# Kernel tuning notes

Hardware: AMD Instinct MI355X
Metric: run time of the kernel (lower is better)

Reference implementation:

```python
import jax, jax.numpy as jnp
import numpy as np

GAMMA = 0.99
LMBDA = 0.95
SHAPE = (8192, 256, 4, 1)  # (batch, steps, agents, 1)


def setup_inputs() -> dict:
    key = jax.random.key(0)
    k1, k2, k3, k4 = jax.random.split(key, 4)
    reward = jax.random.normal(k1, SHAPE, dtype=jnp.float32)
    # sparse binary termination flags (as float, matching terminated.float())
    terminated = (jax.random.uniform(k2, SHAPE) < 0.01).astype(jnp.float32)
    value = jax.random.normal(k3, SHAPE, dtype=jnp.float32)
    next_value = jax.random.normal(k4, SHAPE, dtype=jnp.float32)
    return {"reward": reward, "terminated": terminated,
            "value": value, "next_value": next_value}


def _gae(reward, terminated, value, next_value):
    not_done = 1.0 - terminated
    # delta_t = r_t + gamma * V(s_{t+1}) * not_done_t - V(s_t), all steps at once
    delta = reward + GAMMA * next_value * not_done - value  # (B, T, ...)

    # time-major for the scan: (T, B, ...)
    delta_t = jnp.moveaxis(delta, 1, 0)
    nd_t = jnp.moveaxis(not_done, 1, 0)

    def step(gae, x):
        d, nd = x
        gae = d + GAMMA * LMBDA * nd * gae
        return gae, gae

    init = jnp.zeros(delta_t.shape[1:], dtype=delta.dtype)
    # reverse=True: backward-time recurrence, outputs aligned to original order
    _, adv_t = jax.lax.scan(step, init, (delta_t, nd_t), reverse=True)
    advantages = jnp.moveaxis(adv_t, 0, 1)  # back to (B, T, ...)
    returns = advantages + value
    return advantages, returns


def reference(reward, terminated, value, next_value):
    return _gae(reward, terminated, value, next_value)
```

## Files before the change

### kernel.cpp

```cpp
#include <hip/hip_runtime.h>


#define GAMMA 0.99f
#define LMBDA 0.95f

typedef float f32x4 __attribute__((ext_vector_type(4)));
typedef unsigned char u8;

constexpr float K0 = GAMMA * LMBDA;

__device__ __forceinline__ void issue_loads(
    const f32x4* __restrict__ R4, const f32x4* __restrict__ T4,
    const f32x4* __restrict__ V4, const f32x4* __restrict__ N4,
    int b, int lane, f32x4 r[4], f32x4 tm[4], f32x4 v[4], f32x4 nv[4])
{
#pragma unroll
    for (int q = 0; q < 4; ++q) {
        const int gi = b * 256 + 64 * q + lane;
        r[q]  = R4[gi];
        tm[q] = T4[gi];
        v[q]  = V4[gi];
        nv[q] = N4[gi];
    }
}

__device__ __forceinline__ void phaseA(
    float* __restrict__ D_, u8* __restrict__ C_, int lane,
    const f32x4 r[4], const f32x4 tm[4], const f32x4 nv[4], const f32x4 v[4])
{
#pragma unroll
    for (int q = 0; q < 4; ++q) {
        const int f    = 64 * q + lane;
        const int s    = 255 - f;
        const int row  = s & 15;
        const int col  = (4 * (s >> 4) + 4 * row) & 63;
        const int addr = row * 64 + col;

        f32x4 d4;
        d4.x = r[q].x + GAMMA * nv[q].x * (1.0f - tm[q].x) - v[q].x;
        d4.y = r[q].y + GAMMA * nv[q].y * (1.0f - tm[q].y) - v[q].y;
        d4.z = r[q].z + GAMMA * nv[q].z * (1.0f - tm[q].z) - v[q].z;
        d4.w = r[q].w + GAMMA * nv[q].w * (1.0f - tm[q].w) - v[q].w;
        const unsigned pk = (tm[q].x == 0.0f ? 0x00000001u : 0u)
                          | (tm[q].y == 0.0f ? 0x00000100u : 0u)
                          | (tm[q].z == 0.0f ? 0x00010000u : 0u)
                          | (tm[q].w == 0.0f ? 0x01000000u : 0u);
        *((f32x4*)&D_[addr])    = d4;
        *((unsigned*)&C_[addr]) = pk;
    }
}

__device__ __forceinline__ void scan_store(
    float* __restrict__ D_, const u8* __restrict__ C_,
    int lane, int b, const f32x4 v4[4],
    f32x4* __restrict__ adv4, f32x4* __restrict__ ret4)
{
    asm volatile("s_waitcnt lgkmcnt(0)" ::: "memory");

    const int tc = lane >> 2;
    const int a  = lane & 3;

    float d[16];
    unsigned mask = 0;
#pragma unroll
    for (int j = 0; j < 16; ++j) {
        const int col = (4 * tc + 4 * j + a) & 63;
        d[j] = D_[j * 64 + col];
        mask |= ((unsigned)C_[j * 64 + col]) << j;
    }

    float D = d[0];
    float K = (mask & 1u) ? K0 : 0.0f;
#pragma unroll
    for (int j = 1; j < 16; ++j) {
        const float cj = ((mask >> j) & 1u) ? K0 : 0.0f;
        D = d[j] + cj * D;
        K = cj * K;
    }

#pragma unroll
    for (int s2 = 1; s2 < 16; s2 <<= 1) {
        const float pD = __shfl_up(D, (unsigned)(4 * s2), 64);
        const float pK = __shfl_up(K, (unsigned)(4 * s2), 64);
        if (tc >= s2) { D = D + K * pD; K = K * pK; }
    }

    float x = __shfl_up(D, 4u, 64);
    if (tc == 0) x = 0.0f;

    float g = x;
#pragma unroll
    for (int j = 0; j < 16; ++j) {
        const float cj = ((mask >> j) & 1u) ? K0 : 0.0f;
        g = d[j] + cj * g;
        const int col = (4 * tc + 4 * j + a) & 63;
        D_[j * 64 + col] = g;
    }
    asm volatile("s_waitcnt lgkmcnt(0)" ::: "memory");

#pragma unroll
    for (int q = 0; q < 4; ++q) {
        const int f   = 64 * q + lane;
        const int s   = 255 - f;
        const int row = s & 15;
        const int col = (4 * (s >> 4) + 4 * row) & 63;
        const f32x4 g4 = *((const f32x4*)&D_[row * 64 + col]);

        const int gi = b * 256 + f;
        adv4[gi] = g4;
        ret4[gi] = g4 + v4[q];
    }
    asm volatile("" ::: "memory");
}

__global__ __launch_bounds__(256, 2) void gae_scan_kernel(
    const float* __restrict__ reward,
    const float* __restrict__ terminated,
    const float* __restrict__ value,
    const float* __restrict__ next_value,
    float* __restrict__ adv_out,
    float* __restrict__ ret_out)
{
    __shared__ float bufD[4][16 * 64];
    __shared__ u8    bufC[4][16 * 64];

    const int w    = threadIdx.x >> 6;
    const int lane = threadIdx.x & 63;
    const int wv   = blockIdx.x * 4 + w;

    float* __restrict__ D_ = bufD[w];
    u8*    __restrict__ C_ = bufC[w];

    const f32x4* R4 = (const f32x4*)reward;
    const f32x4* T4 = (const f32x4*)terminated;
    const f32x4* V4 = (const f32x4*)value;
    const f32x4* N4 = (const f32x4*)next_value;
    f32x4* adv4 = (f32x4*)adv_out;
    f32x4* ret4 = (f32x4*)ret_out;

    f32x4 r[2][4], tm[2][4], v[2][4], nv[2][4];

    issue_loads(R4, T4, V4, N4, wv, lane, r[0], tm[0], v[0], nv[0]);

#pragma unroll
    for (int g = 0; g < 4; ++g) {
        const int cb = g & 1;
        const int nb = cb ^ 1;
        const int b  = g * 2048 + wv;

        phaseA(D_, C_, lane, r[cb], tm[cb], nv[cb], v[cb]);

        if (g < 3) {
            issue_loads(R4, T4, V4, N4, b + 2048, lane,
                        r[nb], tm[nb], v[nb], nv[nb]);
        }

        scan_store(D_, C_, lane, b, v[cb], adv4, ret4);
    }
}

extern "C" void kernel_launch(void* const* d_in, const int* in_sizes, int n_in,
                              void* d_out, int out_size, void* d_ws, size_t ws_size,
                              hipStream_t stream) {
    const float* reward     = (const float*)d_in[0];
    const float* terminated = (const float*)d_in[1];
    const float* value      = (const float*)d_in[2];
    const float* next_value = (const float*)d_in[3];

    const int B = 8192;
    const int n_elem = B * 256 * 4;
    float* adv = (float*)d_out;
    float* ret = adv + n_elem;

    gae_scan_kernel<<<512, 256, 0, stream>>>(reward, terminated, value,
                                             next_value, adv, ret);
}
```

Baseline: 176.5 us.

## Split each sequence's time scan across two wavefronts with a shared-memory carry

Each batch sequence is now handled by two wavefronts, each owning half of the 256 time steps, instead of one wavefront scanning all of them. The later-time half hands its aggregate carry to the earlier half through shared memory after a block barrier. The grid doubles to 1024 blocks and launch bounds ask for 4 blocks per CU. Per-wave register and LDS use is halved to raise occupancy and memory-level parallelism, at the cost of a block-wide barrier per iteration and an extra carry exchange.

Measured after the change: 178.2 us. No clear change (+1.0%).

```diff
diff --git a/kernel.cpp b/kernel.cpp
--- a/kernel.cpp
+++ b/kernel.cpp
@@ -9,111 +9,7 @@
 
 constexpr float K0 = GAMMA * LMBDA;
 
-__device__ __forceinline__ void issue_loads(
-    const f32x4* __restrict__ R4, const f32x4* __restrict__ T4,
-    const f32x4* __restrict__ V4, const f32x4* __restrict__ N4,
-    int b, int lane, f32x4 r[4], f32x4 tm[4], f32x4 v[4], f32x4 nv[4])
-{
-#pragma unroll
-    for (int q = 0; q < 4; ++q) {
-        const int gi = b * 256 + 64 * q + lane;
-        r[q]  = R4[gi];
-        tm[q] = T4[gi];
-        v[q]  = V4[gi];
-        nv[q] = N4[gi];
-    }
-}
-
-__device__ __forceinline__ void phaseA(
-    float* __restrict__ D_, u8* __restrict__ C_, int lane,
-    const f32x4 r[4], const f32x4 tm[4], const f32x4 nv[4], const f32x4 v[4])
-{
-#pragma unroll
-    for (int q = 0; q < 4; ++q) {
-        const int f    = 64 * q + lane;
-        const int s    = 255 - f;
-        const int row  = s & 15;
-        const int col  = (4 * (s >> 4) + 4 * row) & 63;
-        const int addr = row * 64 + col;
-
-        f32x4 d4;
-        d4.x = r[q].x + GAMMA * nv[q].x * (1.0f - tm[q].x) - v[q].x;
-        d4.y = r[q].y + GAMMA * nv[q].y * (1.0f - tm[q].y) - v[q].y;
-        d4.z = r[q].z + GAMMA * nv[q].z * (1.0f - tm[q].z) - v[q].z;
-        d4.w = r[q].w + GAMMA * nv[q].w * (1.0f - tm[q].w) - v[q].w;
-        const unsigned pk = (tm[q].x == 0.0f ? 0x00000001u : 0u)
-                          | (tm[q].y == 0.0f ? 0x00000100u : 0u)
-                          | (tm[q].z == 0.0f ? 0x00010000u : 0u)
-                          | (tm[q].w == 0.0f ? 0x01000000u : 0u);
-        *((f32x4*)&D_[addr])    = d4;
-        *((unsigned*)&C_[addr]) = pk;
-    }
-}
-
-__device__ __forceinline__ void scan_store(
-    float* __restrict__ D_, const u8* __restrict__ C_,
-    int lane, int b, const f32x4 v4[4],
-    f32x4* __restrict__ adv4, f32x4* __restrict__ ret4)
-{
-    asm volatile("s_waitcnt lgkmcnt(0)" ::: "memory");
-
-    const int tc = lane >> 2;
-    const int a  = lane & 3;
-
-    float d[16];
-    unsigned mask = 0;
-#pragma unroll
-    for (int j = 0; j < 16; ++j) {
-        const int col = (4 * tc + 4 * j + a) & 63;
-        d[j] = D_[j * 64 + col];
-        mask |= ((unsigned)C_[j * 64 + col]) << j;
-    }
-
-    float D = d[0];
-    float K = (mask & 1u) ? K0 : 0.0f;
-#pragma unroll
-    for (int j = 1; j < 16; ++j) {
-        const float cj = ((mask >> j) & 1u) ? K0 : 0.0f;
-        D = d[j] + cj * D;
-        K = cj * K;
-    }
-
-#pragma unroll
-    for (int s2 = 1; s2 < 16; s2 <<= 1) {
-        const float pD = __shfl_up(D, (unsigned)(4 * s2), 64);
-        const float pK = __shfl_up(K, (unsigned)(4 * s2), 64);
-        if (tc >= s2) { D = D + K * pD; K = K * pK; }
-    }
-
-    float x = __shfl_up(D, 4u, 64);
-    if (tc == 0) x = 0.0f;
-
-    float g = x;
-#pragma unroll
-    for (int j = 0; j < 16; ++j) {
-        const float cj = ((mask >> j) & 1u) ? K0 : 0.0f;
-        g = d[j] + cj * g;
-        const int col = (4 * tc + 4 * j + a) & 63;
-        D_[j * 64 + col] = g;
-    }
-    asm volatile("s_waitcnt lgkmcnt(0)" ::: "memory");
-
-#pragma unroll
-    for (int q = 0; q < 4; ++q) {
-        const int f   = 64 * q + lane;
-        const int s   = 255 - f;
-        const int row = s & 15;
-        const int col = (4 * (s >> 4) + 4 * row) & 63;
-        const f32x4 g4 = *((const f32x4*)&D_[row * 64 + col]);
-
-        const int gi = b * 256 + f;
-        adv4[gi] = g4;
-        ret4[gi] = g4 + v4[q];
-    }
-    asm volatile("" ::: "memory");
-}
-
-__global__ __launch_bounds__(256, 2) void gae_scan_kernel(
+__global__ __launch_bounds__(256, 4) void gae_scan_kernel(
     const float* __restrict__ reward,
     const float* __restrict__ terminated,
     const float* __restrict__ value,
@@ -121,12 +17,15 @@
     float* __restrict__ adv_out,
     float* __restrict__ ret_out)
 {
-    __shared__ float bufD[4][16 * 64];
-    __shared__ u8    bufC[4][16 * 64];
+    __shared__ float bufD[4][8 * 64];
+    __shared__ u8    bufC[4][8 * 64];
+    __shared__ float carryBuf[2][2][4];
 
     const int w    = threadIdx.x >> 6;
     const int lane = threadIdx.x & 63;
-    const int wv   = blockIdx.x * 4 + w;
+    const int sl   = w >> 1;
+    const int h    = w & 1;
+    const int tb   = (1 - h) * 128;
 
     float* __restrict__ D_ = bufD[w];
     u8*    __restrict__ C_ = bufC[w];
@@ -138,24 +37,127 @@
     f32x4* adv4 = (f32x4*)adv_out;
     f32x4* ret4 = (f32x4*)ret_out;
 
-    f32x4 r[2][4], tm[2][4], v[2][4], nv[2][4];
+    const int tc = lane >> 2;
+    const int a  = lane & 3;
 
-    issue_loads(R4, T4, V4, N4, wv, lane, r[0], tm[0], v[0], nv[0]);
+    const int seq0 = blockIdx.x * 2 + sl;
+
+    f32x4 r[2][2], tm[2][2], v[2][2], nv[2][2];
+
+#pragma unroll
+    for (int q = 0; q < 2; ++q) {
+        const int gi = seq0 * 256 + tb + 64 * q + lane;
+        r[0][q]  = R4[gi];
+        tm[0][q] = T4[gi];
+        v[0][q]  = V4[gi];
+        nv[0][q] = N4[gi];
+    }
 
 #pragma unroll
     for (int g = 0; g < 4; ++g) {
         const int cb = g & 1;
         const int nb = cb ^ 1;
-        const int b  = g * 2048 + wv;
+        const int b  = g * 2048 + seq0;
 
-        phaseA(D_, C_, lane, r[cb], tm[cb], nv[cb], v[cb]);
+#pragma unroll
+        for (int q = 0; q < 2; ++q) {
+            const int fl   = 64 * q + lane;
+            const int s    = 127 - fl;
+            const int row  = s & 7;
+            const int tcq  = s >> 3;
+            const int col  = (4 * tcq + 4 * row) & 63;
+            const int addr = row * 64 + col;
+
+            f32x4 d4;
+            d4.x = r[cb][q].x + GAMMA * nv[cb][q].x * (1.0f - tm[cb][q].x) - v[cb][q].x;
+            d4.y = r[cb][q].y + GAMMA * nv[cb][q].y * (1.0f - tm[cb][q].y) - v[cb][q].y;
+            d4.z = r[cb][q].z + GAMMA * nv[cb][q].z * (1.0f - tm[cb][q].z) - v[cb][q].z;
+            d4.w = r[cb][q].w + GAMMA * nv[cb][q].w * (1.0f - tm[cb][q].w) - v[cb][q].w;
+            const unsigned pk = (tm[cb][q].x == 0.0f ? 0x00000001u : 0u)
+                              | (tm[cb][q].y == 0.0f ? 0x00000100u : 0u)
+                              | (tm[cb][q].z == 0.0f ? 0x00010000u : 0u)
+                              | (tm[cb][q].w == 0.0f ? 0x01000000u : 0u);
+            *((f32x4*)&D_[addr])    = d4;
+            *((unsigned*)&C_[addr]) = pk;
+        }
 
         if (g < 3) {
-            issue_loads(R4, T4, V4, N4, b + 2048, lane,
-                        r[nb], tm[nb], v[nb], nv[nb]);
+#pragma unroll
+            for (int q = 0; q < 2; ++q) {
+                const int gi = (b + 2048) * 256 + tb + 64 * q + lane;
+                r[nb][q]  = R4[gi];
+                tm[nb][q] = T4[gi];
+                v[nb][q]  = V4[gi];
+                nv[nb][q] = N4[gi];
+            }
         }
 
-        scan_store(D_, C_, lane, b, v[cb], adv4, ret4);
+        asm volatile("s_waitcnt lgkmcnt(0)" ::: "memory");
+
+        float d[8];
+        unsigned mask = 0;
+#pragma unroll
+        for (int j = 0; j < 8; ++j) {
+            const int col = (4 * tc + 4 * j + a) & 63;
+            d[j] = D_[j * 64 + col];
+            mask |= ((unsigned)C_[j * 64 + col]) << j;
+        }
+
+        float D = d[0];
+        float K = (mask & 1u) ? K0 : 0.0f;
+#pragma unroll
+        for (int j = 1; j < 8; ++j) {
+            const float cj = ((mask >> j) & 1u) ? K0 : 0.0f;
+            D = d[j] + cj * D;
+            K = cj * K;
+        }
+
+#pragma unroll
+        for (int s2 = 1; s2 < 16; s2 <<= 1) {
+            const float pD = __shfl_up(D, (unsigned)(4 * s2), 64);
+            const float pK = __shfl_up(K, (unsigned)(4 * s2), 64);
+            if (tc >= s2) { D = D + K * pD; K = K * pK; }
+        }
+
+        const float Dprev = __shfl_up(D, 4u, 64);
+        const float Kprev = __shfl_up(K, 4u, 64);
+
+        if (h == 0 && tc == 15) carryBuf[cb][sl][a] = D;
+        asm volatile("s_waitcnt lgkmcnt(0)" ::: "memory");
+        __builtin_amdgcn_sched_barrier(0);
+        __builtin_amdgcn_s_barrier();
+
+        float cr = 0.0f;
+        if (h == 1) cr = carryBuf[cb][sl][a];
+
+        float x;
+        if (tc == 0) x = cr;
+        else         x = Dprev + Kprev * cr;
+
+        float gg = x;
+#pragma unroll
+        for (int j = 0; j < 8; ++j) {
+            const float cj = ((mask >> j) & 1u) ? K0 : 0.0f;
+            gg = d[j] + cj * gg;
+            const int col = (4 * tc + 4 * j + a) & 63;
+            D_[j * 64 + col] = gg;
+        }
+        asm volatile("s_waitcnt lgkmcnt(0)" ::: "memory");
+
+#pragma unroll
+        for (int q = 0; q < 2; ++q) {
+            const int fl  = 64 * q + lane;
+            const int s   = 127 - fl;
+            const int row = s & 7;
+            const int tcq = s >> 3;
+            const int col = (4 * tcq + 4 * row) & 63;
+            const f32x4 g4 = *((const f32x4*)&D_[row * 64 + col]);
+
+            const int gi = b * 256 + tb + fl;
+            adv4[gi] = g4;
+            ret4[gi] = g4 + v[cb][q];
+        }
+        asm volatile("" ::: "memory");
     }
 }
 
@@ -172,6 +174,6 @@
     float* adv = (float*)d_out;
     float* ret = adv + n_elem;
 
-    gae_scan_kernel<<<512, 256, 0, stream>>>(reward, terminated, value,
-                                             next_value, adv, ret);
+    gae_scan_kernel<<<1024, 256, 0, stream>>>(reward, terminated, value,
+                                              next_value, adv, ret);
 }
```
